# Kernel tuning notes

Hardware: AMD Instinct MI355X
Metric: run time of the kernel (lower is better)

Reference implementation:

```python
import jax, jax.numpy as jnp
import numpy as np

E = 512
H = 8
DH = E // H
LN_EPS = 1e-5


def setup_inputs() -> dict:
    key = jax.random.key(0)
    ks = jax.random.split(key, 8)
    s = 1.0 / np.sqrt(E)
    return {
        "query": jax.random.normal(ks[0], (2, 2048, E), jnp.float32),
        "key_value": jax.random.normal(ks[1], (2, 4096, E), jnp.float32),
        "Wq": jax.random.normal(ks[2], (E, E), jnp.float32) * s,
        "bq": jnp.zeros((E,), jnp.float32),
        "Wk": jax.random.normal(ks[3], (E, E), jnp.float32) * s,
        "bk": jnp.zeros((E,), jnp.float32),
        "Wv": jax.random.normal(ks[4], (E, E), jnp.float32) * s,
        "bv": jnp.zeros((E,), jnp.float32),
        "Wo": jax.random.normal(ks[5], (E, E), jnp.float32) * s,
        "bo": jnp.zeros((E,), jnp.float32),
        "ln_gamma": jnp.ones((E,), jnp.float32),
        "ln_beta": jnp.zeros((E,), jnp.float32),
    }


def reference(query, key_value, Wq, bq, Wk, bk, Wv, bv, Wo, bo, ln_gamma, ln_beta):
    B, Lq, _ = query.shape
    Lk = key_value.shape[1]
    # Projections (torch Linear: x @ W.T + b)
    q = (query @ Wq.T + bq).reshape(B, Lq, H, DH)
    k = (key_value @ Wk.T + bk).reshape(B, Lk, H, DH)
    v = (key_value @ Wv.T + bv).reshape(B, Lk, H, DH)
    scale = 1.0 / np.sqrt(DH).astype(np.float32)
    scores = jnp.einsum("bqhd,bkhd->bhqk", q, k) * scale  # [B,H,Lq,Lk]
    attn = jax.nn.softmax(scores, axis=-1)
    ctx = jnp.einsum("bhqk,bkhd->bqhd", attn, v).reshape(B, Lq, E)
    attn_out = ctx @ Wo.T + bo
    # residual + LayerNorm (dropout is identity in eval)
    x = query + attn_out
    mu = jnp.mean(x, axis=-1, keepdims=True)
    var = jnp.mean(jnp.square(x - mu), axis=-1, keepdims=True)
    return (x - mu) * jax.lax.rsqrt(var + LN_EPS) * ln_gamma + ln_beta
```

## Files before the change

kernel.cpp:

```cpp
#include <hip/hip_runtime.h>
#include <hip/hip_bf16.h>

typedef __bf16 bf16;
typedef __bf16 bf16x8 __attribute__((ext_vector_type(8)));
typedef __bf16 bf16x4 __attribute__((ext_vector_type(4)));
typedef float f32x4 __attribute__((ext_vector_type(4)));
typedef float f32x16 __attribute__((ext_vector_type(16)));
typedef unsigned int u32x4 __attribute__((ext_vector_type(4)));

#define MFMA16(a, b, c) __builtin_amdgcn_mfma_f32_16x16x32_bf16((a), (b), (c), 0, 0, 0)
#define MFMA32(a, b, c) __builtin_amdgcn_mfma_f32_32x32x16_bf16((a), (b), (c), 0, 0, 0)

constexpr int LQ = 2048, LK = 4096, E = 512, H = 8, DH = 64;
#define QSCALE 0.1803368801111137f

#if __has_builtin(__builtin_amdgcn_exp2f)
#define EXP2(x) __builtin_amdgcn_exp2f(x)
#else
#define EXP2(x) __expf(0.6931471805599453f * (x))
#endif

__device__ __forceinline__ bf16x8 ld8(const bf16* p) { return *(const bf16x8*)p; }

__global__ __launch_bounds__(256) void cvt4_kernel(
    const float* __restrict__ w0, const float* __restrict__ w1,
    const float* __restrict__ w2, const float* __restrict__ w3,
    bf16* __restrict__ dst) {
  const float* srcs[4] = {w0, w1, w2, w3};
  const float* src = srcs[blockIdx.y];
  bf16* d = dst + (size_t)blockIdx.y * 262144;
  int i = (blockIdx.x * 256 + threadIdx.x) * 4;
  f32x4 v = *(const f32x4*)(src + i);
  bf16x4 o;
  for (int j = 0; j < 4; ++j) o[j] = (bf16)v[j];
  *(bf16x4*)(d + i) = o;
}

__global__ __launch_bounds__(256) void proj_gemm_kernel(
    const float* __restrict__ query, const float* __restrict__ kv,
    const bf16* __restrict__ Wall,
    const float* __restrict__ bq, const float* __restrict__ bk,
    const float* __restrict__ bv,
    bf16* __restrict__ qproj, bf16* __restrict__ kproj, bf16* __restrict__ vt) {
  __shared__ bf16 smA[2][128][72];
  __shared__ bf16 smB[2][128][72];
  const int tid = threadIdx.x;
  const int lane = tid & 63, wave = tid >> 6;
  const int lrow = lane & 15, quad = lane >> 4;
  const int wm = wave & 1, wn = wave >> 1;

  int x = blockIdx.x, z, mt;
  if (x < 32) { z = 0; mt = x; }
  else if (x < 96) { z = 1; mt = x - 32; }
  else { z = 2; mt = x - 96; }
  const float* A = ((z == 0) ? query : kv) + (size_t)mt * 128 * E;
  const bf16* W = Wall + (size_t)z * 262144;
  const float* bias = (z == 0) ? bq : (z == 1) ? bk : bv;
  const int n0 = blockIdx.y * 128;

  const int arow = tid >> 4, acol = tid & 15;
  const int brow = tid >> 3, bcol = tid & 7;

  f32x4 pa[8];
  bf16x8 pb[4];
#define LOAD_T(t)                                                             \
  {                                                                           \
    for (int p = 0; p < 8; ++p)                                               \
      pa[p] = *(const f32x4*)(A + (size_t)(p * 16 + arow) * E + (t) * 64 +    \
                              acol * 4);                                      \
    for (int p = 0; p < 4; ++p)                                               \
      pb[p] = ld8(W + (size_t)(n0 + p * 32 + brow) * E + (t) * 64 + bcol * 8);\
  }
#define STORE_T(bs)                                                           \
  {                                                                           \
    for (int p = 0; p < 8; ++p) {                                             \
      bf16x4 av;                                                              \
      for (int e = 0; e < 4; ++e) av[e] = (bf16)pa[p][e];                     \
      *(bf16x4*)&smA[bs][p * 16 + arow][acol * 4] = av;                       \
    }                                                                         \
    for (int p = 0; p < 4; ++p)                                               \
      *(bf16x8*)&smB[bs][p * 32 + brow][bcol * 8] = pb[p];                    \
  }

  LOAD_T(0);
  STORE_T(0);
  LOAD_T(1);
  __syncthreads();

  f32x4 acc[4][4] = {};
  for (int t = 0; t < 8; ++t) {
    const int bs = t & 1;
    bf16x8 af[2][4], bfr[2][4];
    for (int ks = 0; ks < 2; ++ks)
      for (int i = 0; i < 4; ++i)
        af[ks][i] = ld8(&smA[bs][wm * 64 + 16 * i + lrow][ks * 32 + quad * 8]);
    for (int ks = 0; ks < 2; ++ks)
      for (int c = 0; c < 4; ++c)
        bfr[ks][c] = ld8(&smB[bs][wn * 64 + 16 * c + lrow][ks * 32 + quad * 8]);
    for (int ks = 0; ks < 2; ++ks)
      for (int i = 0; i < 4; ++i)
        for (int c = 0; c < 4; ++c)
          acc[i][c] = MFMA16(af[ks][i], bfr[ks][c], acc[i][c]);
    if (t < 7) {
      STORE_T(bs ^ 1);
      if (t < 6) LOAD_T(t + 2);
    }
    __syncthreads();
  }
#undef LOAD_T
#undef STORE_T

  const float qsc = (z == 0) ? QSCALE : 1.f;
  float bvl[4];
  for (int c = 0; c < 4; ++c) bvl[c] = bias[n0 + wn * 64 + 16 * c + lrow];
  bf16* Cs = &smA[0][0][0];
  for (int i = 0; i < 4; ++i)
    for (int c = 0; c < 4; ++c)
      for (int r = 0; r < 4; ++r) {
        int row = wm * 64 + 16 * i + 4 * quad + r;
        int col = wn * 64 + 16 * c + lrow;
        bf16 val = (bf16)((acc[i][c][r] + bvl[c]) * qsc);
        if (z < 2) Cs[row * 136 + col] = val;
        else       Cs[col * 136 + row] = val;
      }
  __syncthreads();
  const int rr = tid >> 1, hh = tid & 1;
  if (z < 2) {
    bf16* Y = (z == 0) ? qproj : kproj;
    bf16* dstp = Y + (size_t)(mt * 128 + rr) * E + n0 + hh * 64;
    for (int j = 0; j < 8; ++j)
      *(bf16x8*)(dstp + j * 8) = *(bf16x8*)&Cs[rr * 136 + hh * 64 + j * 8];
  } else {
    int m0g = mt * 128, b = m0g >> 12, kk0 = m0g & 4095;
    int ng = n0 + rr, hd = ng >> 6, d = ng & 63;
    bf16* dstp = vt + ((size_t)((b * 8 + hd) * 64 + d)) * LK + kk0 + hh * 64;
    for (int j = 0; j < 8; ++j)
      *(bf16x8*)(dstp + j * 8) = *(bf16x8*)&Cs[rr * 136 + hh * 64 + j * 8];
  }
}

__global__ __launch_bounds__(256, 2) void attn_kernel(
    const bf16* __restrict__ qp, const bf16* __restrict__ kp,
    const bf16* __restrict__ vtg, bf16* __restrict__ ctx) {
  const int tid = threadIdx.x;
  const int lane = tid & 63, wave = tid >> 6;
  const int l31 = lane & 31, hi = lane >> 5;
  const int hw = blockIdx.x;
  const int xcd = hw & 7, ii = hw >> 3;
  const int bh = xcd * 2 + (ii >> 5), qt = ii & 31;
  const int b = bh >> 3, h = bh & 7;
  const int q0 = qt * 64;

  __shared__ __align__(16) char smem[70656];

  bf16x8 qf[2][4];
  for (int t = 0; t < 2; ++t)
    for (int st = 0; st < 4; ++st)
      qf[t][st] = ld8(qp + (size_t)(b * LQ + q0 + 32 * t + l31) * E + h * DH +
                      st * 16 + hi * 8);

  float lp[2] = {0.f, 0.f};
  f32x16 acc[2][2] = {};

  const int kkbase = wave * 1024;
  const bf16* kfb =
      kp + ((size_t)b * LK + kkbase + l31) * E + h * DH + hi * 8;
  const bf16* vfb = vtg + ((size_t)bh * DH + l31) * LK + kkbase + hi * 8;

#define LOADT(kf_, vf_, it)                                          \
  {                                                                  \
    const bf16* kpp = kfb + (size_t)(it) * 32 * E;                   \
    kf_[0] = ld8(kpp);                                               \
    kf_[1] = ld8(kpp + 16);                                          \
    kf_[2] = ld8(kpp + 32);                                          \
    kf_[3] = ld8(kpp + 48);                                          \
    const bf16* vpp = vfb + (it) * 32;                               \
    vf_[0] = ld8(vpp);                                               \
    vf_[1] = ld8(vpp + 16);                                          \
    vf_[2] = ld8(vpp + (size_t)32 * LK);                             \
    vf_[3] = ld8(vpp + (size_t)32 * LK + 16);                        \
  }

#define COMPUTE(kf_, vf_)                                            \
  _Pragma("unroll")                                                  \
  for (int t = 0; t < 2; ++t) {                                      \
    f32x16 s_ = {};                                                  \
    __builtin_amdgcn_s_setprio(1);                                   \
    s_ = MFMA32(kf_[0], qf[t][0], s_);                               \
    s_ = MFMA32(kf_[1], qf[t][1], s_);                               \
    s_ = MFMA32(kf_[2], qf[t][2], s_);                               \
    s_ = MFMA32(kf_[3], qf[t][3], s_);                               \
    __builtin_amdgcn_s_setprio(0);                                   \
    unsigned w_[4][2];                                               \
    _Pragma("unroll")                                                \
    for (int t4 = 0; t4 < 4; ++t4)                                   \
      _Pragma("unroll")                                              \
      for (int u = 0; u < 2; ++u) {                                  \
        float e0 = EXP2(s_[4 * t4 + 2 * u]);                         \
        float e1 = EXP2(s_[4 * t4 + 2 * u + 1]);                     \
        lp[t] += e0;                                                 \
        lp[t] += e1;                                                 \
        asm("v_cvt_pk_bf16_f32 %0, %1, %2"                           \
            : "=v"(w_[t4][u])                                        \
            : "v"(e0), "v"(e1));                                     \
      }                                                              \
    bf16x8 paf[2];                                                   \
    _Pragma("unroll")                                                \
    for (int s = 0; s < 2; ++s) {                                    \
      unsigned a0 = w_[2 * s][0], b0 = w_[2 * s + 1][0];             \
      unsigned a1 = w_[2 * s][1], b1 = w_[2 * s + 1][1];             \
      asm("v_permlane32_swap_b32 %0, %1" : "+v"(a0), "+v"(b0));      \
      asm("v_permlane32_swap_b32 %0, %1" : "+v"(a1), "+v"(b1));      \
      u32x4 pw_ = {a0, a1, b0, b1};                                  \
      paf[s] = *(bf16x8*)&pw_;                                       \
    }                                                                \
    __builtin_amdgcn_s_setprio(1);                                   \
    acc[t][0] = MFMA32(paf[0], vf_[0], acc[t][0]);                   \
    acc[t][0] = MFMA32(paf[1], vf_[1], acc[t][0]);                   \
    acc[t][1] = MFMA32(paf[0], vf_[2], acc[t][1]);                   \
    acc[t][1] = MFMA32(paf[1], vf_[3], acc[t][1]);                   \
    __builtin_amdgcn_s_setprio(0);                                   \
  }

  bf16x8 kfA[4], vfA[4], kfB[4], vfB[4];
  LOADT(kfA, vfA, 0);
  for (int it = 0; it < 32; it += 2) {
    LOADT(kfB, vfB, it + 1);
    COMPUTE(kfA, vfA);
    if (it + 2 < 32) LOADT(kfA, vfA, it + 2);
    COMPUTE(kfB, vfB);
  }
#undef LOADT
#undef COMPUTE

  for (int t = 0; t < 2; ++t) lp[t] += __shfl_xor(lp[t], 32);

  __syncthreads();
  float* F = (float*)smem;
  float* Lr = (float*)(smem + 69632);
#pragma unroll
  for (int t = 0; t < 2; ++t)
    for (int dt = 0; dt < 2; ++dt)
#pragma unroll
      for (int r = 0; r < 16; ++r) {
        int q = 32 * t + (r & 3) + 8 * (r >> 2) + 4 * hi;
        F[(wave * 64 + q) * 68 + dt * 32 + l31] = acc[t][dt][r];
      }
  if (hi == 0) {
    Lr[wave * 64 + l31] = lp[0];
    Lr[wave * 64 + 32 + l31] = lp[1];
  }
  __syncthreads();
  {
    const int q = tid >> 2, d0 = (tid & 3) * 16;
    float ls = Lr[q] + Lr[64 + q] + Lr[128 + q] + Lr[192 + q];
    float inv = 1.f / ls;
    float o[16] = {};
    for (int w2 = 0; w2 < 4; ++w2) {
      const float* Fr = &F[(w2 * 64 + q) * 68 + d0];
      for (int j = 0; j < 16; j += 4) {
        f32x4 x = *(const f32x4*)(Fr + j);
        o[j] += x[0];
        o[j + 1] += x[1];
        o[j + 2] += x[2];
        o[j + 3] += x[3];
      }
    }
    bf16* dst = ctx + (size_t)(b * LQ + q0 + q) * E + h * DH + d0;
    bf16x8 ov0, ov1;
    for (int j = 0; j < 8; ++j) {
      ov0[j] = (bf16)(o[j] * inv);
      ov1[j] = (bf16)(o[8 + j] * inv);
    }
    *(bf16x8*)dst = ov0;
    *(bf16x8*)(dst + 8) = ov1;
  }
}

__global__ __launch_bounds__(512) void outln_kernel(
    const bf16* __restrict__ Cx, const bf16* __restrict__ Wo,
    const float* __restrict__ bo, const float* __restrict__ resid,
    const float* __restrict__ gamma, const float* __restrict__ beta,
    float* __restrict__ out) {
  const int tid = threadIdx.x;
  const int lane = tid & 63, wave = tid >> 6;
  const int lrow = lane & 15, quad = lane >> 4;
  const int m0 = blockIdx.x * 16;
  const int n0 = wave * 64;

  __shared__ bf16 As[16][520];
  __shared__ bf16 Wos[512][72];
  __shared__ float red1[16][8], red2[16][8];
  {
    int r = tid >> 5, ch = tid & 31;
    const bf16* src = Cx + (size_t)(m0 + r) * E + ch * 16;
    *(bf16x8*)&As[r][ch * 16] = ld8(src);
    *(bf16x8*)&As[r][ch * 16 + 8] = ld8(src + 8);
  }
  const int wr = tid >> 3, wc = tid & 7;
  bf16x8 pw[8];
  for (int p = 0; p < 8; ++p)
    pw[p] = ld8(Wo + (size_t)(p * 64 + wr) * E + wc * 8);
  __syncthreads();

  f32x4 acc[4] = {};
  for (int t = 0; t < 8; ++t) {
    for (int p = 0; p < 8; ++p)
      *(bf16x8*)&Wos[p * 64 + wr][wc * 8] = pw[p];
    __syncthreads();
    if (t < 7)
      for (int p = 0; p < 8; ++p)
        pw[p] = ld8(Wo + (size_t)(p * 64 + wr) * E + (t + 1) * 64 + wc * 8);
    for (int ks = 0; ks < 2; ++ks) {
      bf16x8 a = *(const bf16x8*)&As[lrow][t * 64 + ks * 32 + quad * 8];
      for (int c = 0; c < 4; ++c) {
        bf16x8 w = *(const bf16x8*)&Wos[n0 + 16 * c + lrow][ks * 32 + quad * 8];
        acc[c] = MFMA16(a, w, acc[c]);
      }
    }
    __syncthreads();
  }

  float s1[4] = {}, s2[4] = {};
  for (int c = 0; c < 4; ++c) {
    int n = n0 + 16 * c + lrow;
    float bb = bo[n];
    for (int r = 0; r < 4; ++r) {
      int m = 4 * quad + r;
      float xv = acc[c][r] + bb + resid[(size_t)(m0 + m) * E + n];
      acc[c][r] = xv;
      s1[r] += xv;
      s2[r] += xv * xv;
    }
  }
  for (int off = 1; off < 16; off <<= 1)
    for (int r = 0; r < 4; ++r) {
      s1[r] += __shfl_xor(s1[r], off);
      s2[r] += __shfl_xor(s2[r], off);
    }
  if (lrow == 0)
    for (int r = 0; r < 4; ++r) {
      red1[4 * quad + r][wave] = s1[r];
      red2[4 * quad + r][wave] = s2[r];
    }
  __syncthreads();
  float mu[4], rstd[4];
  for (int r = 0; r < 4; ++r) {
    int m = 4 * quad + r;
    float t1 = 0.f, t2 = 0.f;
    for (int w = 0; w < 8; ++w) { t1 += red1[m][w]; t2 += red2[m][w]; }
    float mean = t1 * (1.f / 512.f);
    float var = t2 * (1.f / 512.f) - mean * mean;
    mu[r] = mean;
    rstd[r] = rsqrtf(var + 1e-5f);
  }
  for (int c = 0; c < 4; ++c) {
    int n = n0 + 16 * c + lrow;
    float gm = gamma[n], bt = beta[n];
    for (int r = 0; r < 4; ++r) {
      int m = m0 + 4 * quad + r;
      out[(size_t)m * E + n] = (acc[c][r] - mu[r]) * rstd[r] * gm + bt;
    }
  }
}

extern "C" void kernel_launch(void* const* d_in, const int* in_sizes, int n_in,
                              void* d_out, int out_size, void* d_ws, size_t ws_size,
                              hipStream_t stream) {
  const float* query     = (const float*)d_in[0];
  const float* key_value = (const float*)d_in[1];
  const float* Wq = (const float*)d_in[2];
  const float* bq = (const float*)d_in[3];
  const float* Wk = (const float*)d_in[4];
  const float* bk = (const float*)d_in[5];
  const float* Wv = (const float*)d_in[6];
  const float* bv = (const float*)d_in[7];
  const float* Wo = (const float*)d_in[8];
  const float* bo = (const float*)d_in[9];
  const float* gamma = (const float*)d_in[10];
  const float* beta  = (const float*)d_in[11];
  float* out = (float*)d_out;

  bf16* Wb    = (bf16*)d_ws;
  bf16* Wob   = Wb + (size_t)3 * 262144;
  bf16* qproj = Wb + (size_t)4 * 262144;
  bf16* kproj = qproj + (size_t)4096 * 512;
  bf16* vt    = kproj + (size_t)8192 * 512;

  cvt4_kernel<<<dim3(256, 4), 256, 0, stream>>>(Wq, Wk, Wv, Wo, Wb);
  proj_gemm_kernel<<<dim3(160, 4), 256, 0, stream>>>(
      query, key_value, Wb, bq, bk, bv, qproj, kproj, vt);
  attn_kernel<<<512, 256, 0, stream>>>(qproj, kproj, vt, qproj );
  outln_kernel<<<256, 512, 0, stream>>>(qproj, Wob, bo, query, gamma, beta, out);
}
```

Measured before the change: 193.4 us.

## Store K and V in MFMA fragment-tiled layout and halve attention LDS reduction

The projection kernel now writes K and V in a per-head layout tiled to match the MFMA fragment order, so each lane's attention loads are contiguous 16-byte chunks with wide coalescing instead of strided rows across E or LK. The attention epilogue reduces the cross-wave partial outputs in two halves of the head dimension, which cuts LDS use from about 70KB to 35KB. This can allow more resident blocks, at the cost of an extra barrier round and scalar, non-vector LDS reads. The V write-out in the projection kernel becomes more scattered.

After: 165.4 us. -14.5%, faster.

```diff
diff --git a/kernel.cpp b/kernel.cpp
--- a/kernel.cpp
+++ b/kernel.cpp
@@ -125,23 +125,35 @@
       }
   __syncthreads();
   const int rr = tid >> 1, hh = tid & 1;
-  if (z < 2) {
-    bf16* Y = (z == 0) ? qproj : kproj;
-    bf16* dstp = Y + (size_t)(mt * 128 + rr) * E + n0 + hh * 64;
+  if (z == 0) {
+    bf16* dstp = qproj + (size_t)(mt * 128 + rr) * E + n0 + hh * 64;
     for (int j = 0; j < 8; ++j)
       *(bf16x8*)(dstp + j * 8) = *(bf16x8*)&Cs[rr * 136 + hh * 64 + j * 8];
+  } else if (z == 1) {
+    int mtg = mt * 128 + rr;
+    int b2 = mtg >> 12, kk = mtg & 4095;
+    int t32 = kk >> 5, l31 = kk & 31;
+    int bh2 = b2 * 8 + (n0 >> 6) + hh;
+    bf16* dstp = kproj + (size_t)bh2 * 262144 + (size_t)t32 * 2048 + l31 * 8;
+    for (int j = 0; j < 8; ++j)
+      *(bf16x8*)(dstp + j * 256) = *(bf16x8*)&Cs[rr * 136 + hh * 64 + j * 8];
   } else {
-    int m0g = mt * 128, b = m0g >> 12, kk0 = m0g & 4095;
+    int m0g = mt * 128, b2 = m0g >> 12, kk0 = m0g & 4095;
     int ng = n0 + rr, hd = ng >> 6, d = ng & 63;
-    bf16* dstp = vt + ((size_t)((b * 8 + hd) * 64 + d)) * LK + kk0 + hh * 64;
-    for (int j = 0; j < 8; ++j)
-      *(bf16x8*)(dstp + j * 8) = *(bf16x8*)&Cs[rr * 136 + hh * 64 + j * 8];
+    int bh2 = b2 * 8 + hd, dt = d >> 5, l31 = d & 31;
+    bf16* dstp = vt + (size_t)bh2 * 262144 + dt * 1024 + l31 * 8;
+    for (int j = 0; j < 8; ++j) {
+      int kk = kk0 + hh * 64 + 8 * j;
+      int t32 = kk >> 5, s = (kk >> 4) & 1, hi2 = (kk >> 3) & 1;
+      *(bf16x8*)(dstp + (size_t)t32 * 2048 + s * 512 + hi2 * 256) =
+          *(bf16x8*)&Cs[rr * 136 + hh * 64 + j * 8];
+    }
   }
 }
 
 __global__ __launch_bounds__(256, 2) void attn_kernel(
-    const bf16* __restrict__ qp, const bf16* __restrict__ kp,
-    const bf16* __restrict__ vtg, bf16* __restrict__ ctx) {
+    const bf16* __restrict__ qp, const bf16* __restrict__ kfg,
+    const bf16* __restrict__ vfg, bf16* __restrict__ ctx) {
   const int tid = threadIdx.x;
   const int lane = tid & 63, wave = tid >> 6;
   const int l31 = lane & 31, hi = lane >> 5;
@@ -151,7 +163,7 @@
   const int b = bh >> 3, h = bh & 7;
   const int q0 = qt * 64;
 
-  __shared__ __align__(16) char smem[70656];
+  __shared__ __align__(16) char smem[34816];
 
   bf16x8 qf[2][4];
   for (int t = 0; t < 2; ++t)
@@ -162,23 +174,22 @@
   float lp[2] = {0.f, 0.f};
   f32x16 acc[2][2] = {};
 
-  const int kkbase = wave * 1024;
-  const bf16* kfb =
-      kp + ((size_t)b * LK + kkbase + l31) * E + h * DH + hi * 8;
-  const bf16* vfb = vtg + ((size_t)bh * DH + l31) * LK + kkbase + hi * 8;
+  const size_t tb = ((size_t)bh * 128 + wave * 32) * 2048;
+  const bf16* kb = kfg + tb + hi * 256 + l31 * 8;
+  const bf16* vb = vfg + tb + hi * 256 + l31 * 8;
 
 #define LOADT(kf_, vf_, it)                                          \
   {                                                                  \
-    const bf16* kpp = kfb + (size_t)(it) * 32 * E;                   \
-    kf_[0] = ld8(kpp);                                               \
-    kf_[1] = ld8(kpp + 16);                                          \
-    kf_[2] = ld8(kpp + 32);                                          \
-    kf_[3] = ld8(kpp + 48);                                          \
-    const bf16* vpp = vfb + (it) * 32;                               \
-    vf_[0] = ld8(vpp);                                               \
-    vf_[1] = ld8(vpp + 16);                                          \
-    vf_[2] = ld8(vpp + (size_t)32 * LK);                             \
-    vf_[3] = ld8(vpp + (size_t)32 * LK + 16);                        \
+    const bf16* kp_ = kb + (size_t)(it) * 2048;                      \
+    kf_[0] = ld8(kp_);                                               \
+    kf_[1] = ld8(kp_ + 512);                                         \
+    kf_[2] = ld8(kp_ + 1024);                                        \
+    kf_[3] = ld8(kp_ + 1536);                                        \
+    const bf16* vp_ = vb + (size_t)(it) * 2048;                      \
+    vf_[0] = ld8(vp_);                                               \
+    vf_[1] = ld8(vp_ + 512);                                         \
+    vf_[2] = ld8(vp_ + 1024);                                        \
+    vf_[3] = ld8(vp_ + 1536);                                        \
   }
 
 #define COMPUTE(kf_, vf_)                                            \
@@ -235,45 +246,53 @@
 
   for (int t = 0; t < 2; ++t) lp[t] += __shfl_xor(lp[t], 32);
 
-  __syncthreads();
   float* F = (float*)smem;
-  float* Lr = (float*)(smem + 69632);
-#pragma unroll
-  for (int t = 0; t < 2; ++t)
-    for (int dt = 0; dt < 2; ++dt)
-#pragma unroll
-      for (int r = 0; r < 16; ++r) {
-        int q = 32 * t + (r & 3) + 8 * (r >> 2) + 4 * hi;
-        F[(wave * 64 + q) * 68 + dt * 32 + l31] = acc[t][dt][r];
-      }
+  float* Lr = (float*)(smem + 33792);
   if (hi == 0) {
     Lr[wave * 64 + l31] = lp[0];
     Lr[wave * 64 + 32 + l31] = lp[1];
   }
-  __syncthreads();
+#pragma unroll
+  for (int t = 0; t < 2; ++t)
+#pragma unroll
+    for (int r = 0; r < 16; ++r) {
+      int q = 32 * t + (r & 3) + 8 * (r >> 2) + 4 * hi;
+      F[(wave * 64 + q) * 33 + l31] = acc[t][0][r];
+    }
+  __syncthreads();
+  const int mq = tid >> 2, d0 = (tid & 3) * 8;
+  float ls = Lr[mq] + Lr[64 + mq] + Lr[128 + mq] + Lr[192 + mq];
+  const float inv = 1.f / ls;
   {
-    const int q = tid >> 2, d0 = (tid & 3) * 16;
-    float ls = Lr[q] + Lr[64 + q] + Lr[128 + q] + Lr[192 + q];
-    float inv = 1.f / ls;
-    float o[16] = {};
+    float o[8] = {};
+#pragma unroll
     for (int w2 = 0; w2 < 4; ++w2) {
-      const float* Fr = &F[(w2 * 64 + q) * 68 + d0];
-      for (int j = 0; j < 16; j += 4) {
-        f32x4 x = *(const f32x4*)(Fr + j);
-        o[j] += x[0];
-        o[j + 1] += x[1];
-        o[j + 2] += x[2];
-        o[j + 3] += x[3];
-      }
-    }
-    bf16* dst = ctx + (size_t)(b * LQ + q0 + q) * E + h * DH + d0;
-    bf16x8 ov0, ov1;
-    for (int j = 0; j < 8; ++j) {
-      ov0[j] = (bf16)(o[j] * inv);
-      ov1[j] = (bf16)(o[8 + j] * inv);
-    }
-    *(bf16x8*)dst = ov0;
-    *(bf16x8*)(dst + 8) = ov1;
+      const float* Fr = &F[(w2 * 64 + mq) * 33 + d0];
+      for (int j = 0; j < 8; ++j) o[j] += Fr[j];
+    }
+    bf16x8 ov;
+    for (int j = 0; j < 8; ++j) ov[j] = (bf16)(o[j] * inv);
+    *(bf16x8*)(ctx + (size_t)(b * LQ + q0 + mq) * E + h * DH + d0) = ov;
+  }
+  __syncthreads();
+#pragma unroll
+  for (int t = 0; t < 2; ++t)
+#pragma unroll
+    for (int r = 0; r < 16; ++r) {
+      int q = 32 * t + (r & 3) + 8 * (r >> 2) + 4 * hi;
+      F[(wave * 64 + q) * 33 + l31] = acc[t][1][r];
+    }
+  __syncthreads();
+  {
+    float o[8] = {};
+#pragma unroll
+    for (int w2 = 0; w2 < 4; ++w2) {
+      const float* Fr = &F[(w2 * 64 + mq) * 33 + d0];
+      for (int j = 0; j < 8; ++j) o[j] += Fr[j];
+    }
+    bf16x8 ov;
+    for (int j = 0; j < 8; ++j) ov[j] = (bf16)(o[j] * inv);
+    *(bf16x8*)(ctx + (size_t)(b * LQ + q0 + mq) * E + h * DH + 32 + d0) = ov;
   }
 }
 
```
